# Optimization experiments

Hardware: AMD Instinct MI355X
Metric: run time of the kernel (lower is better)

The kernel has to match this reference:

```python
import jax, jax.numpy as jnp
import numpy as np

B, N, P = 64, 800000, 128          # batch, total CpG features, n_pathways (capsules)
H1, H2, C = 256, 128, 32           # MLP hidden_topology and n_output
EPS = 1e-5                         # BatchNorm1d eps


def _xavier(key, fan_in, fan_out, shape):
    bound = np.sqrt(6.0 / (fan_in + fan_out))
    return jax.random.uniform(key, shape, jnp.float32, -bound, bound)


def setup_inputs() -> dict:
    key = jax.random.key(0)
    ks = jax.random.split(key, 10)
    x = jax.random.normal(ks[0], (B, N), jnp.float32)
    # idx: sorted pathway assignment, equal capsule sizes N//P (matches module_lens)
    idx = jnp.sort(jax.random.randint(ks[1], (N,), 0, P)).astype(jnp.int64)
    # SPWModulesLayer.weight: xavier_uniform on shape (1, N)
    w = _xavier(ks[2], N, 1, (N,))
    co_w = jax.random.uniform(ks[3], (P,), jnp.float32, 0.0, 4.0)  # CancelOut init
    bn0_g, bn0_b = jnp.ones(P, jnp.float32), jnp.zeros(P, jnp.float32)
    W1, b1 = _xavier(ks[4], P, H1, (P, H1)), jnp.zeros(H1, jnp.float32)
    bn1_g, bn1_b = jnp.ones(H1, jnp.float32), jnp.zeros(H1, jnp.float32)
    W2, b2 = _xavier(ks[5], H1, H2, (H1, H2)), jnp.zeros(H2, jnp.float32)
    bn2_g, bn2_b = jnp.ones(H2, jnp.float32), jnp.zeros(H2, jnp.float32)
    Wo, bo = _xavier(ks[6], H2, C, (H2, C)), jnp.zeros(C, jnp.float32)
    return {"x": x, "w": w, "co_w": co_w,
            "bn0_g": bn0_g, "bn0_b": bn0_b,
            "W1": W1, "b1": b1, "bn1_g": bn1_g, "bn1_b": bn1_b,
            "W2": W2, "b2": b2, "bn2_g": bn2_g, "bn2_b": bn2_b,
            "Wo": Wo, "bo": bo, "idx": idx}


def _bn(z, g, b):
    # BatchNorm1d in training mode: batch mean, biased variance
    m = jnp.mean(z, axis=0)
    v = jnp.mean((z - m) ** 2, axis=0)
    return (z - m) * jax.lax.rsqrt(v + EPS) * g + b


def reference(x, w, co_w, bn0_g, bn0_b, W1, b1, bn1_g, bn1_b,
              W2, b2, bn2_g, bn2_b, Wo, bo, idx):
    # --- SPWModulesLayer: weighted scatter_add over pathway index (last dim) ---
    WX = jnp.zeros((x.shape[0], P), x.dtype).at[:, idx].add(x * w)   # [B, P]
    Z = _bn(jax.nn.relu(WX), bn0_g, bn0_b)                           # ReLU + BN
    Z = Z * jax.nn.sigmoid(co_w)                                     # CancelOut
    # --- MLP head: Linear->ReLU->BN twice, then Linear->Softmax ---
    h = _bn(jax.nn.relu(Z @ W1 + b1), bn1_g, bn1_b)
    h = _bn(jax.nn.relu(h @ W2 + b2), bn2_g, bn2_b)
    y = jax.nn.softmax(h @ Wo + bo, axis=-1)
    return (y, Z)
```

## Files before the change

### kernel.cpp

```cpp
#include <hip/hip_runtime.h>
#include <hip/hip_bf16.h>
#include <type_traits>

#define BB     64
#define NF4    200000
#define CHUNKS 3125
#define NP     128
#define NH1    256
#define NH2    128
#define NC     32
#define EPSV   1e-5f

typedef float fx4 __attribute__((ext_vector_type(4)));

#define AS_G __attribute__((address_space(1)))
#define AS_L __attribute__((address_space(3)))

__device__ __forceinline__ float dot4(fx4 a, fx4 b) {
    return fmaf(a[0], b[0], fmaf(a[1], b[1], fmaf(a[2], b[2], a[3] * b[3])));
}

template <int N, int I = 0, typename F>
__device__ __forceinline__ void static_for(F&& f) {
    if constexpr (I < N) {
        f(std::integral_constant<int, I>{});
        static_for<N, I + 1>(f);
    }
}

__device__ __forceinline__ int bitrev3(int l) {
    return ((l & 1) << 2) | (l & 2) | ((l & 4) >> 2);
}

template <int C, int M>
__device__ __forceinline__ void red_step(float* v, int lane) {
    const bool hi = (lane & M) != 0;
    #pragma unroll
    for (int j = 0; j < C / 2; ++j) {
        float mine  = hi ? v[j + C / 2] : v[j];
        float other = hi ? v[j]         : v[j + C / 2];
        v[j] = mine + __shfl_xor(other, M);
    }
}

__device__ __forceinline__ void reduce_emit8(float* acc, int lane, int b0,
                                             int path, float* __restrict__ WX) {
    red_step<8, 1>(acc, lane);
    red_step<4, 2>(acc, lane);
    red_step<2, 4>(acc, lane);
    float s = acc[0];
    s += __shfl_xor(s, 8);
    s += __shfl_xor(s, 16);
    s += __shfl_xor(s, 32);
    if (lane < 8)
        atomicAdd(&WX[(b0 + bitrev3(lane)) * NP + path], s);
}

__global__ __launch_bounds__(256) void k_scatter(
    const float* __restrict__ x, const float* __restrict__ w,
    const int* __restrict__ idx, float* __restrict__ WX)
{
    __shared__ fx4 lds4[32 * 64];
    const int tid  = threadIdx.x;
    const int lane = tid & 63;
    const int wq   = tid >> 6;
    const int wid  = blockIdx.x;
    const int ch   = wid >> 1;
    const int b0   = ((wid & 1) << 5) + wq * 8;
    const int n4   = ch * 64 + lane;

    const fx4*  __restrict__ w4 = reinterpret_cast<const fx4*>(w);
    const int4* __restrict__ p4 = reinterpret_cast<const int4*>(idx);
    const fx4*  __restrict__ x4 = reinterpret_cast<const fx4*>(x);

    const fx4  wv = w4[n4];
    const int4 pv = p4[n4];
    const int  pLo = __builtin_amdgcn_readfirstlane(pv.x);
    const int  pHi = __shfl(pv.w, 63);
    const bool uniform = (pLo == pHi);

    fx4 wLo, wHi;
    wLo[0] = (pv.x == pLo) ? wv[0] : 0.f;  wHi[0] = (pv.x == pHi) ? wv[0] : 0.f;
    wLo[1] = (pv.y == pLo) ? wv[1] : 0.f;  wHi[1] = (pv.y == pHi) ? wv[1] : 0.f;
    wLo[2] = (pv.z == pLo) ? wv[2] : 0.f;  wHi[2] = (pv.z == pHi) ? wv[2] : 0.f;
    wLo[3] = (pv.w == pLo) ? wv[3] : 0.f;  wHi[3] = (pv.w == pHi) ? wv[3] : 0.f;

    fx4* const myl = lds4 + wq * 8 * 64;

    static_for<8>([&](auto I) {
        constexpr int i = I.value;
        const float* gp = (const float*)(x4 + ((size_t)(b0 + i) * NF4 + n4));
        __builtin_amdgcn_global_load_lds((const AS_G float*)gp,
                                         (AS_L float*)(myl + i * 64), 16, 0, 0);
    });
    asm volatile("s_waitcnt vmcnt(0)" ::: "memory");

    if (uniform) {
        float acc[8];
        static_for<8>([&](auto I) {
            constexpr int i = I.value;
            acc[i] = dot4(myl[i * 64 + lane], wLo);
        });
        reduce_emit8(acc, lane, b0, pLo, WX);
    } else {
        float acc[8], accH[8];
        static_for<8>([&](auto I) {
            constexpr int i = I.value;
            const fx4 xr = myl[i * 64 + lane];
            acc[i]  = dot4(xr, wLo);
            accH[i] = dot4(xr, wHi);
        });
        reduce_emit8(acc,  lane, b0, pLo, WX);
        reduce_emit8(accH, lane, b0, pHi, WX);
    }
}

__global__ void k_zero(float* __restrict__ WX)
{
    const int i = blockIdx.x * 256 + threadIdx.x;
    if (i < BB * NP) WX[i] = 0.f;
}

__device__ __forceinline__ float bn_shfl(float a, float gj, float bj)
{
    float s = a, q = a * a;
    #pragma unroll
    for (int off = 32; off > 0; off >>= 1) {
        s += __shfl_xor(s, off);
        q += __shfl_xor(q, off);
    }
    const float m   = s * (1.f / BB);
    const float var = q * (1.f / BB) - m * m;
    return (a - m) * rsqrtf(var + EPSV) * gj + bj;
}

__global__ __launch_bounds__(256) void k_fc1z(
    const float* __restrict__ WX,   const float* __restrict__ co_w,
    const float* __restrict__ bn0g, const float* __restrict__ bn0b,
    const float* __restrict__ W1,   const float* __restrict__ b1,
    const float* __restrict__ bn1g, const float* __restrict__ bn1b,
    float* __restrict__ Zout, float* __restrict__ h1t)
{
    __shared__ float Zl[NP * 65];
    const int tid  = threadIdx.x;
    const int wv   = tid >> 6;
    const int lane = tid & 63;
    const int blk  = blockIdx.x;

    if (tid < NP) {
        const int p = tid;
        float sum = 0.f, sq = 0.f;
        #pragma unroll 8
        for (int b = 0; b < BB; ++b) {
            const float r = fmaxf(WX[b * NP + p], 0.f);
            sum += r; sq += r * r;
        }
        const float m   = sum * (1.f / BB);
        const float var = sq * (1.f / BB) - m * m;
        const float sc  = rsqrtf(var + EPSV) * bn0g[p];
        const float bt  = bn0b[p];
        const float sig = 1.f / (1.f + expf(-co_w[p]));
        #pragma unroll 8
        for (int b = 0; b < BB; ++b) {
            const float r = fmaxf(WX[b * NP + p], 0.f);
            const float z = ((r - m) * sc + bt) * sig;
            Zl[p * 65 + b] = z;
            if (blk == 0) Zout[b * NP + p] = z;
        }
    }
    __syncthreads();

    const int j = blk * 4 + wv;
    float acc = b1[j];
    #pragma unroll 8
    for (int k = 0; k < NP; ++k)
        acc = fmaf(Zl[k * 65 + lane], W1[k * NH1 + j], acc);
    h1t[j * BB + lane] = bn_shfl(fmaxf(acc, 0.f), bn1g[j], bn1b[j]);
}

template <int K, int NOUT>
__global__ void k_fc_bn_t(const float* __restrict__ in_t,
                          const float* __restrict__ W,
                          const float* __restrict__ bias,
                          const float* __restrict__ g,
                          const float* __restrict__ beta,
                          float* __restrict__ out_t)
{
    const int j = blockIdx.x;
    const int b = threadIdx.x;
    float acc = bias[j];
    #pragma unroll 8
    for (int k = 0; k < K; ++k)
        acc = fmaf(in_t[k * BB + b], W[k * NOUT + j], acc);
    out_t[j * BB + b] = bn_shfl(fmaxf(acc, 0.f), g[j], beta[j]);
}

__global__ void k_head(const float* __restrict__ h2t,
                       const float* __restrict__ Wo,
                       const float* __restrict__ bo,
                       float* __restrict__ y)
{
    const int b = blockIdx.x;
    const int c = threadIdx.x;
    float acc = bo[c];
    #pragma unroll 8
    for (int k = 0; k < NH2; ++k)
        acc = fmaf(h2t[k * BB + b], Wo[k * NC + c], acc);
    float mx = acc;
    #pragma unroll
    for (int off = 16; off > 0; off >>= 1)
        mx = fmaxf(mx, __shfl_xor(mx, off));
    const float e = expf(acc - mx);
    float s = e;
    #pragma unroll
    for (int off = 16; off > 0; off >>= 1)
        s += __shfl_xor(s, off);
    y[b * NC + c] = e / s;
}

extern "C" void kernel_launch(void* const* d_in, const int* in_sizes, int n_in,
                              void* d_out, int out_size, void* d_ws, size_t ws_size,
                              hipStream_t stream)
{
    const float* x    = (const float*)d_in[0];
    const float* w    = (const float*)d_in[1];
    const float* co_w = (const float*)d_in[2];
    const float* bn0g = (const float*)d_in[3];
    const float* bn0b = (const float*)d_in[4];
    const float* W1   = (const float*)d_in[5];
    const float* b1   = (const float*)d_in[6];
    const float* bn1g = (const float*)d_in[7];
    const float* bn1b = (const float*)d_in[8];
    const float* W2   = (const float*)d_in[9];
    const float* b2   = (const float*)d_in[10];
    const float* bn2g = (const float*)d_in[11];
    const float* bn2b = (const float*)d_in[12];
    const float* Wo   = (const float*)d_in[13];
    const float* bo   = (const float*)d_in[14];
    const int*   idx  = (const int*)d_in[15];

    float* out = (float*)d_out;
    float* y   = out;
    float* Z   = out + BB * NC;

    float* WX  = (float*)d_ws;
    float* h1t = WX + BB * NP;
    float* h2t = h1t + BB * NH1;

    k_zero<<<32, 256, 0, stream>>>(WX);
    k_scatter<<<CHUNKS * 2, 256, 0, stream>>>(x, w, idx, WX);
    k_fc1z<<<64, 256, 0, stream>>>(WX, co_w, bn0g, bn0b,
                                   W1, b1, bn1g, bn1b, Z, h1t);
    k_fc_bn_t<NH1, NH2><<<NH2, BB, 0, stream>>>(h1t, W2, b2, bn2g, bn2b, h2t);
    k_head<<<BB, NC, 0, stream>>>(h2t, Wo, bo, y);
}
```

Before: 84.23 us.

## Make each scatter wave loop over all batches with double-buffered LDS DMA

The scatter kernel now gives each wave one feature chunk and has it walk all 64 batch rows in 8 steps, instead of spreading one chunk over 8 waves. Loads go straight to LDS through a double buffer with explicit vmcnt waits, so the next rows load while the current ones are reduced. The weight and index loads are amortised over more work and there are far fewer blocks. The cost is much less memory-level parallelism per wave and fewer waves in flight overall, and the hand-tuned waitcnt counts are fragile.

```diff
diff --git a/kernel.cpp b/kernel.cpp
--- a/kernel.cpp
+++ b/kernel.cpp
@@ -1,6 +1,5 @@
 #include <hip/hip_runtime.h>
 #include <hip/hip_bf16.h>
-#include <type_traits>
 
 #define BB     64
 #define NF4    200000
@@ -20,14 +19,6 @@
     return fmaf(a[0], b[0], fmaf(a[1], b[1], fmaf(a[2], b[2], a[3] * b[3])));
 }
 
-template <int N, int I = 0, typename F>
-__device__ __forceinline__ void static_for(F&& f) {
-    if constexpr (I < N) {
-        f(std::integral_constant<int, I>{});
-        static_for<N, I + 1>(f);
-    }
-}
-
 __device__ __forceinline__ int bitrev3(int l) {
     return ((l & 1) << 2) | (l & 2) | ((l & 4) >> 2);
 }
@@ -43,8 +34,7 @@
     }
 }
 
-__device__ __forceinline__ void reduce_emit8(float* acc, int lane, int b0,
-                                             int path, float* __restrict__ WX) {
+__device__ __forceinline__ float reduce8(float* acc, int lane) {
     red_step<8, 1>(acc, lane);
     red_step<4, 2>(acc, lane);
     red_step<2, 4>(acc, lane);
@@ -52,21 +42,19 @@
     s += __shfl_xor(s, 8);
     s += __shfl_xor(s, 16);
     s += __shfl_xor(s, 32);
-    if (lane < 8)
-        atomicAdd(&WX[(b0 + bitrev3(lane)) * NP + path], s);
-}
-
-__global__ __launch_bounds__(256) void k_scatter(
+    return s;
+}
+
+__global__ __launch_bounds__(128) void k_scatter(
     const float* __restrict__ x, const float* __restrict__ w,
     const int* __restrict__ idx, float* __restrict__ WX)
 {
-    __shared__ fx4 lds4[32 * 64];
+    __shared__ fx4 lds4[2 * 2 * 8 * 64];
     const int tid  = threadIdx.x;
     const int lane = tid & 63;
-    const int wq   = tid >> 6;
-    const int wid  = blockIdx.x;
-    const int ch   = wid >> 1;
-    const int b0   = ((wid & 1) << 5) + wq * 8;
+    const int q    = tid >> 6;
+    const int ch   = blockIdx.x * 2 + q;
+    if (ch >= CHUNKS) return;
     const int n4   = ch * 64 + lane;
 
     const fx4*  __restrict__ w4 = reinterpret_cast<const fx4*>(w);
@@ -85,33 +73,60 @@
     wLo[2] = (pv.z == pLo) ? wv[2] : 0.f;  wHi[2] = (pv.z == pHi) ? wv[2] : 0.f;
     wLo[3] = (pv.w == pLo) ? wv[3] : 0.f;  wHi[3] = (pv.w == pHi) ? wv[3] : 0.f;
 
-    fx4* const myl = lds4 + wq * 8 * 64;
-
-    static_for<8>([&](auto I) {
-        constexpr int i = I.value;
-        const float* gp = (const float*)(x4 + ((size_t)(b0 + i) * NF4 + n4));
-        __builtin_amdgcn_global_load_lds((const AS_G float*)gp,
-                                         (AS_L float*)(myl + i * 64), 16, 0, 0);
-    });
-    asm volatile("s_waitcnt vmcnt(0)" ::: "memory");
-
-    if (uniform) {
-        float acc[8];
-        static_for<8>([&](auto I) {
-            constexpr int i = I.value;
-            acc[i] = dot4(myl[i * 64 + lane], wLo);
-        });
-        reduce_emit8(acc, lane, b0, pLo, WX);
-    } else {
+    fx4* const base = lds4 + q * (2 * 8 * 64);
+
+    auto dma = [&](int o) {
+        const int s = o & 1;
+        #pragma unroll
+        for (int i = 0; i < 8; ++i) {
+            const float* gp = (const float*)(x4 + ((size_t)(o * 8 + i) * NF4 + n4));
+            __builtin_amdgcn_global_load_lds((const AS_G float*)gp,
+                                             (AS_L float*)(base + (s * 8 + i) * 64),
+                                             16, 0, 0);
+        }
+    };
+
+    dma(0); dma(1);
+
+    #pragma unroll
+    for (int o = 0; o < 8; ++o) {
+        if (o == 0)      asm volatile("s_waitcnt vmcnt(8)" ::: "memory");
+        else if (o < 7)  asm volatile("s_waitcnt vmcnt(9)" ::: "memory");
+        else             asm volatile("s_waitcnt vmcnt(1)" ::: "memory");
+
+        const int s = o & 1;
+        fx4 xr[8];
+        #pragma unroll
+        for (int i = 0; i < 8; ++i) {
+            const unsigned laddr =
+                (unsigned)(size_t)(AS_L char*)(base + (s * 8 + i) * 64 + lane);
+            asm volatile("ds_read_b128 %0, %1" : "=v"(xr[i]) : "v"(laddr));
+        }
+        asm volatile("s_waitcnt lgkmcnt(0)" ::: "memory");
+        __builtin_amdgcn_sched_barrier(0);
+
         float acc[8], accH[8];
-        static_for<8>([&](auto I) {
-            constexpr int i = I.value;
-            const fx4 xr = myl[i * 64 + lane];
-            acc[i]  = dot4(xr, wLo);
-            accH[i] = dot4(xr, wHi);
-        });
-        reduce_emit8(acc,  lane, b0, pLo, WX);
-        reduce_emit8(accH, lane, b0, pHi, WX);
+        #pragma unroll
+        for (int i = 0; i < 8; ++i)
+            acc[i] = dot4(xr[i], wLo);
+        const float sLo = reduce8(acc, lane);
+        float sHi = 0.f;
+        if (!uniform) {
+            #pragma unroll
+            for (int i = 0; i < 8; ++i)
+                accH[i] = dot4(xr[i], wHi);
+            sHi = reduce8(accH, lane);
+        }
+        const int   b0  = o * 8;
+        const float val = (lane < 8) ? sLo : sHi;
+        const int   col = (lane < 8) ? pLo : pHi;
+        const int   nl  = uniform ? 8 : 16;
+        if (lane < nl)
+            atomicAdd(&WX[(b0 + bitrev3(lane & 7)) * NP + col], val);
+
+        __builtin_amdgcn_sched_barrier(0);
+        if (o + 2 < 8) dma(o + 2);
+        __builtin_amdgcn_sched_barrier(0);
     }
 }
 
@@ -248,7 +263,7 @@
     float* h2t = h1t + BB * NH1;
 
     k_zero<<<32, 256, 0, stream>>>(WX);
-    k_scatter<<<CHUNKS * 2, 256, 0, stream>>>(x, w, idx, WX);
+    k_scatter<<<(CHUNKS + 1) / 2, 128, 0, stream>>>(x, w, idx, WX);
     k_fc1z<<<64, 256, 0, stream>>>(WX, co_w, bn0g, bn0b,
                                    W1, b1, bn1g, bn1b, Z, h1t);
     k_fc_bn_t<NH1, NH2><<<NH2, BB, 0, stream>>>(h1t, W2, b2, bn2g, bn2b, h2t);
```

Measured after the change: 85.60 us. Within noise of the previous version (+1.6%).
